# Optimization experiments

Measured on AMD Instinct MI355X. Metric: run time of the kernel, lower is better.

## Reference

```python
import jax, jax.numpy as jnp
import numpy as np

N = 100000
E = 1600000
K = 2  # KProp steps


def setup_inputs() -> dict:
    key = jax.random.key(0)
    ks = jax.random.split(key, 8)
    x = jax.random.normal(ks[0], (N, 64), dtype=jnp.float32)
    edge_index = jax.random.randint(ks[1], (2, E), 0, N, dtype=jnp.int32)
    s = 1.0 / np.sqrt(64)
    W2l = jax.random.normal(ks[2], (64, 64), dtype=jnp.float32) * s
    W2r = jax.random.normal(ks[3], (64, 64), dtype=jnp.float32) * s
    b2 = jnp.zeros((64,), dtype=jnp.float32)
    W3l = jax.random.normal(ks[4], (64, 16), dtype=jnp.float32) * s
    W3r = jax.random.normal(ks[5], (64, 16), dtype=jnp.float32) * s
    b3 = jnp.zeros((16,), dtype=jnp.float32)
    return {"x": x, "edge_index": edge_index, "W2l": W2l, "W2r": W2r,
            "b2": b2, "W3l": W3l, "W3r": W3r, "b3": b3}


def reference(x, edge_index, W2l, W2r, b2, W3l, W3r, b3):
    dst, src = edge_index[0], edge_index[1]  # adj_t[i,j]: edge j -> i
    ones = jnp.ones((E,), dtype=x.dtype)
    deg = jax.ops.segment_sum(ones, dst, num_segments=N)  # in-degree
    dinv = jnp.where(deg > 0, jax.lax.rsqrt(jnp.maximum(deg, 1.0)), 0.0)
    w = dinv[dst] * dinv[src]  # gcn_norm weights (no self-loops in norm)

    # KProp: K steps of (D^-1/2 A D^-1/2 + I) @ h  (set_diag adds unit diag)
    h = x
    for _ in range(K):
        h = jax.ops.segment_sum(w[:, None] * h[src], dst, num_segments=N) + h

    degm = jnp.maximum(deg, 1.0)[:, None]

    # SAGEConv 1: mean-neighbor aggregate + root weight
    agg = jax.ops.segment_sum(h[src], dst, num_segments=N) / degm
    h = agg @ W2l + h @ W2r + b2
    h = jax.nn.selu(h)

    # SAGEConv 2
    agg = jax.ops.segment_sum(h[src], dst, num_segments=N) / degm
    h = agg @ W3l + h @ W3r + b3
    return jax.nn.softmax(h, axis=1)
```

## Files before the change

### kernel.cpp

```cpp
#include <hip/hip_runtime.h>
#include <hip/hip_bf16.h>

#define NNODES 100000
#define NEDGES 1600000
#define NC 25
#define CAP1 68000
#define NBUCK 391
#define BCAP 4800
#define SPLIT_TILE 2048
#define NSPLIT ((NEDGES + SPLIT_TILE - 1) / SPLIT_TILE)
#define T2TILES 17

typedef short short8 __attribute__((ext_vector_type(8)));
typedef unsigned short ushx8 __attribute__((ext_vector_type(8)));
typedef float floatx4 __attribute__((ext_vector_type(4)));

__device__ __forceinline__ unsigned short f2b(float f) {
    unsigned u = __float_as_uint(f);
    u += 0x7fffu + ((u >> 16) & 1u);
    return (unsigned short)(u >> 16);
}

__device__ __forceinline__ void acc8(float* a, ushx8 u) {
#pragma unroll
    for (int i = 0; i < 8; ++i)
        a[i] += __uint_as_float((unsigned)u[i] << 16);
}

__global__ __launch_bounds__(256) void split1_kernel(
    const int* __restrict__ dst, const int* __restrict__ src,
    int* __restrict__ gcur1, unsigned* __restrict__ cpairs) {
    __shared__ int lhist[NC];
    __shared__ int lstart[NC];
    __shared__ int ldst[SPLIT_TILE];
    int t = threadIdx.x;
    if (t < NC) lhist[t] = 0;
    __syncthreads();
    int base = blockIdx.x * SPLIT_TILE;
    int n = min(SPLIT_TILE, NEDGES - base);
    for (int i = t; i < n; i += 256) {
        int d = dst[base + i];
        ldst[i] = d;
        atomicAdd(&lhist[d >> 12], 1);
    }
    __syncthreads();
    if (t < NC) {
        int c = lhist[t];
        lstart[t] = (c > 0) ? atomicAdd(&gcur1[t], c) : 0;
        lhist[t] = 0;
    }
    __syncthreads();
    for (int i = t; i < n; i += 256) {
        int d = ldst[i];
        int k = d >> 12;
        int s = src[base + i];
        int pos = lstart[k] + atomicAdd(&lhist[k], 1);
        cpairs[(size_t)k * CAP1 + pos] = ((unsigned)s << 12) | (unsigned)(d & 4095);
    }
}

__global__ __launch_bounds__(256) void split2_kernel(
    const unsigned* __restrict__ cpairs, const int* __restrict__ gcur1,
    int* __restrict__ gcur2, unsigned* __restrict__ fpairs) {
    int c = blockIdx.x / T2TILES;
    int tile = blockIdx.x % T2TILES;
    int cnt = gcur1[c];
    int base = tile * 4096;
    if (base >= cnt) return;
    int n = min(4096, cnt - base);
    __shared__ unsigned stash[4096];
    __shared__ int lhist[16];
    __shared__ int lstart[16];
    int t = threadIdx.x;
    if (t < 16) lhist[t] = 0;
    __syncthreads();
    const unsigned* pb = cpairs + (size_t)c * CAP1 + base;
    for (int i = t; i < n; i += 256) {
        unsigned p = pb[i];
        stash[i] = p;
        atomicAdd(&lhist[(p >> 8) & 15], 1);
    }
    __syncthreads();
    if (t < 16) {
        int cc = lhist[t];
        lstart[t] = (cc > 0) ? atomicAdd(&gcur2[c * 16 + t], cc) : 0;
        lhist[t] = 0;
    }
    __syncthreads();
    for (int i = t; i < n; i += 256) {
        unsigned p = stash[i];
        int f = (p >> 8) & 15;
        int pos = lstart[f] + atomicAdd(&lhist[f], 1);
        fpairs[(size_t)(c * 16 + f) * BCAP + pos] = ((p >> 12) << 8) | (p & 255u);
    }
}

__global__ void bucketscan_kernel(const int* __restrict__ gcur2, int* __restrict__ basearr) {
    __shared__ int lds[512];
    int t = threadIdx.x;
    int v = (t < NBUCK) ? gcur2[t] : 0;
    lds[t] = v;
    __syncthreads();
    for (int s = 1; s < 512; s <<= 1) {
        int u = (t >= s) ? lds[t - s] : 0;
        __syncthreads();
        lds[t] += u;
        __syncthreads();
    }
    if (t < NBUCK) basearr[t] = lds[t] - v;
}

__global__ __launch_bounds__(256) void finalize_kernel(
    const unsigned* __restrict__ fpairs, const int* __restrict__ gcur2,
    const int* __restrict__ basearr, const float* __restrict__ x,
    int* __restrict__ col, int* __restrict__ deg, int* __restrict__ rowoff,
    float* __restrict__ dinv, unsigned short* __restrict__ g0b) {
    __shared__ int ldeg[256];
    __shared__ int lcur[256];
    __shared__ float ldi[256];
    __shared__ int lsc[256];
    int k = blockIdx.x;
    int t = threadIdx.x;
    int node0 = k << 8;
    int ncount = min(256, NNODES - node0);
    int base = basearr[k];
    int count = gcur2[k];
    ldeg[t] = 0;
    __syncthreads();
    const unsigned* pb = fpairs + (size_t)k * BCAP;
    for (int i = t; i < count; i += 256) {
        atomicAdd(&ldeg[pb[i] & 255], 1);
    }
    __syncthreads();
    int a = ldeg[t];
    lsc[t] = a;
    __syncthreads();
    for (int s = 1; s < 256; s <<= 1) {
        int v = (t >= s) ? lsc[t - s] : 0;
        __syncthreads();
        lsc[t] += v;
        __syncthreads();
    }
    int excl = lsc[t] - a;
    lcur[t] = base + excl;
    if (t < ncount) {
        int n0 = node0 + t;
        rowoff[n0] = base + excl;
        deg[n0] = a;
        float di = (a > 0) ? rsqrtf((float)a) : 0.0f;
        ldi[t] = di;
        dinv[n0] = di;
    }
    __syncthreads();
    for (int i = t; i < count; i += 256) {
        unsigned p = pb[i];
        int dl = (int)(p & 255u);
        int s = (int)(p >> 8);
        int pos = atomicAdd(&lcur[dl], 1);
        col[pos] = s;
    }
    const float4* x4 = (const float4*)x;
    int f4count = ncount * 16;
    int b4 = node0 * 16;
    for (int j = t; j < f4count; j += 256) {
        float di = ldi[j >> 4];
        float4 v = x4[b4 + j];
        ushort4 u;
        u.x = f2b(di * v.x); u.y = f2b(di * v.y);
        u.z = f2b(di * v.z); u.w = f2b(di * v.w);
        *(ushort4*)(g0b + (size_t)(b4 + j) * 4) = u;
    }
}

template <int MODE>
__global__ __launch_bounds__(256) void gatherw_kernel(
    const unsigned short* __restrict__ vin, const float* __restrict__ hinf,
    const unsigned short* __restrict__ hinb,
    unsigned short* __restrict__ out0, unsigned short* __restrict__ out1,
    const int* __restrict__ rowoff, const int* __restrict__ deg,
    const int* __restrict__ col, const float* __restrict__ dinv) {
    int node = blockIdx.x * 4 + (threadIdx.x >> 6);
    int lane = threadIdx.x & 63;
    int sub = lane & 7;
    int g = lane >> 3;
    int beg = rowoff[node];
    int dg = deg[node];
    int end = beg + dg;
    float af[8] = {0.f, 0.f, 0.f, 0.f, 0.f, 0.f, 0.f, 0.f};
    float bf[8] = {0.f, 0.f, 0.f, 0.f, 0.f, 0.f, 0.f, 0.f};
    int e = beg + g;
    for (; e + 8 < end; e += 16) {
        int c0 = col[e];
        int c1 = col[e + 8];
        ushx8 u0 = *(const ushx8*)(vin + (size_t)c0 * 64 + sub * 8);
        ushx8 u1 = *(const ushx8*)(vin + (size_t)c1 * 64 + sub * 8);
        acc8(af, u0);
        acc8(bf, u1);
    }
    if (e < end) {
        int c0 = col[e];
        ushx8 u0 = *(const ushx8*)(vin + (size_t)c0 * 64 + sub * 8);
        acc8(af, u0);
    }
#pragma unroll
    for (int i = 0; i < 8; ++i) {
        float v = af[i] + bf[i];
        v += __shfl_xor(v, 8);
        v += __shfl_xor(v, 16);
        v += __shfl_xor(v, 32);
        af[i] = v;
    }
    if (lane < 8) {
        size_t off = (size_t)node * 64 + lane * 8;
        if (MODE <= 1) {
            float di = dinv[node];
            float hv[8];
            if (MODE == 0) {
                float4 h0 = *(const float4*)(hinf + off);
                float4 h1 = *(const float4*)(hinf + off + 4);
                hv[0] = h0.x; hv[1] = h0.y; hv[2] = h0.z; hv[3] = h0.w;
                hv[4] = h1.x; hv[5] = h1.y; hv[6] = h1.z; hv[7] = h1.w;
            } else {
                ushx8 u = *(const ushx8*)(hinb + off);
#pragma unroll
                for (int i = 0; i < 8; ++i) hv[i] = __uint_as_float((unsigned)u[i] << 16);
            }
            ushx8 uh, ug;
#pragma unroll
            for (int i = 0; i < 8; ++i) {
                float hn = hv[i] + di * af[i];
                uh[i] = f2b(hn);
                if (MODE == 0) ug[i] = f2b(di * hn);
            }
            *(ushx8*)(out0 + off) = uh;
            if (MODE == 0) *(ushx8*)(out1 + off) = ug;
        } else {
            float r = 1.0f / (float)(dg > 0 ? dg : 1);
            ushx8 u;
#pragma unroll
            for (int i = 0; i < 8; ++i) u[i] = f2b(af[i] * r);
            *(ushx8*)(out0 + off) = u;
        }
    }
}

__global__ __launch_bounds__(256) void dense1_mfma(
    const unsigned short* __restrict__ aggb, const unsigned short* __restrict__ hb,
    unsigned short* __restrict__ h3b,
    const float* __restrict__ W2l, const float* __restrict__ W2r,
    const float* __restrict__ b2) {
    __shared__ unsigned short Wt[64 * 144];
    int t = threadIdx.x;
    for (int idx = t; idx < 128 * 64; idx += 256) {
        int k = idx >> 6, j = idx & 63;
        float v = (k < 64) ? W2l[k * 64 + j] : W2r[(k - 64) * 64 + j];
        Wt[j * 144 + k] = f2b(v);
    }
    __syncthreads();
    int wib = t >> 6, lane = t & 63;
    int tile = blockIdx.x * 4 + wib;
    if (tile * 16 >= NNODES) return;
    int node0 = tile * 16;
    int jj = lane & 15, kg = lane >> 4;
    short8 bfrag[4][4];
#pragma unroll
    for (int nt = 0; nt < 4; ++nt)
#pragma unroll
        for (int s = 0; s < 4; ++s)
            bfrag[nt][s] = *(const short8*)&Wt[(nt * 16 + jj) * 144 + s * 32 + kg * 8];
    int arow = node0 + jj;
    const unsigned short* ap = aggb + (size_t)arow * 64 + kg * 8;
    const unsigned short* hp = hb + (size_t)arow * 64 + kg * 8;
    short8 afrag[4];
    afrag[0] = *(const short8*)ap;
    afrag[1] = *(const short8*)(ap + 32);
    afrag[2] = *(const short8*)hp;
    afrag[3] = *(const short8*)(hp + 32);
    const float lam = 1.0507009873554804934193349852946f;
    const float alp = 1.6732632423543772848170429916717f;
#pragma unroll
    for (int nt = 0; nt < 4; ++nt) {
        floatx4 acc = {0.f, 0.f, 0.f, 0.f};
#pragma unroll
        for (int s = 0; s < 4; ++s)
            acc = __builtin_amdgcn_mfma_f32_16x16x32_bf16(afrag[s], bfrag[nt][s], acc, 0, 0, 0);
        float bias = b2[nt * 16 + jj];
#pragma unroll
        for (int r = 0; r < 4; ++r) {
            float v = acc[r] + bias;
            float o = (v > 0.0f) ? lam * v : lam * alp * expm1f(v);
            int node = node0 + kg * 4 + r;
            h3b[(size_t)node * 64 + nt * 16 + jj] = f2b(o);
        }
    }
}

__global__ __launch_bounds__(256) void dense2_mfma(
    const unsigned short* __restrict__ aggb, const unsigned short* __restrict__ hb,
    float* __restrict__ out,
    const float* __restrict__ W3l, const float* __restrict__ W3r,
    const float* __restrict__ b3) {
    __shared__ unsigned short Wt[16 * 144];
    int t = threadIdx.x;
    for (int idx = t; idx < 128 * 16; idx += 256) {
        int k = idx >> 4, j = idx & 15;
        float v = (k < 64) ? W3l[k * 16 + j] : W3r[(k - 64) * 16 + j];
        Wt[j * 144 + k] = f2b(v);
    }
    __syncthreads();
    int wib = t >> 6, lane = t & 63;
    int tile = blockIdx.x * 4 + wib;
    if (tile * 16 >= NNODES) return;
    int node0 = tile * 16;
    int jj = lane & 15, kg = lane >> 4;
    short8 bfrag[4];
#pragma unroll
    for (int s = 0; s < 4; ++s)
        bfrag[s] = *(const short8*)&Wt[jj * 144 + s * 32 + kg * 8];
    int arow = node0 + jj;
    const unsigned short* ap = aggb + (size_t)arow * 64 + kg * 8;
    const unsigned short* hp = hb + (size_t)arow * 64 + kg * 8;
    short8 afrag[4];
    afrag[0] = *(const short8*)ap;
    afrag[1] = *(const short8*)(ap + 32);
    afrag[2] = *(const short8*)hp;
    afrag[3] = *(const short8*)(hp + 32);
    floatx4 acc = {0.f, 0.f, 0.f, 0.f};
#pragma unroll
    for (int s = 0; s < 4; ++s)
        acc = __builtin_amdgcn_mfma_f32_16x16x32_bf16(afrag[s], bfrag[s], acc, 0, 0, 0);
    float bias = b3[jj];
#pragma unroll
    for (int r = 0; r < 4; ++r) {
        float v = acc[r] + bias;
        float m = v;
        m = fmaxf(m, __shfl_xor(m, 1));
        m = fmaxf(m, __shfl_xor(m, 2));
        m = fmaxf(m, __shfl_xor(m, 4));
        m = fmaxf(m, __shfl_xor(m, 8));
        float ex = expf(v - m);
        float s2 = ex;
        s2 += __shfl_xor(s2, 1);
        s2 += __shfl_xor(s2, 2);
        s2 += __shfl_xor(s2, 4);
        s2 += __shfl_xor(s2, 8);
        int node = node0 + kg * 4 + r;
        out[(size_t)node * 16 + jj] = ex / s2;
    }
}

extern "C" void kernel_launch(void* const* d_in, const int* in_sizes, int n_in,
                              void* d_out, int out_size, void* d_ws, size_t ws_size,
                              hipStream_t stream) {
    const float* x   = (const float*)d_in[0];
    const int*   ei  = (const int*)d_in[1];
    const float* W2l = (const float*)d_in[2];
    const float* W2r = (const float*)d_in[3];
    const float* b2  = (const float*)d_in[4];
    const float* W3l = (const float*)d_in[5];
    const float* W3r = (const float*)d_in[6];
    const float* b3  = (const float*)d_in[7];
    float* out = (float*)d_out;

    const int* dst = ei;
    const int* src = ei + NEDGES;

    char* ws = (char*)d_ws;
    unsigned short* B0 = (unsigned short*)ws; ws += (size_t)NNODES * 64 * 2;
    unsigned short* B1 = (unsigned short*)ws; ws += (size_t)NNODES * 64 * 2;
    unsigned short* B2 = (unsigned short*)ws; ws += (size_t)NNODES * 64 * 2;
    int*      col     = (int*)ws;      ws += (size_t)NEDGES * 4;
    int*      deg     = (int*)ws;      ws += (size_t)NNODES * 4;
    int*      rowoff  = (int*)ws;      ws += (size_t)NNODES * 4;
    float*    dinv    = (float*)ws;    ws += (size_t)NNODES * 4;
    int*      gcur1   = (int*)ws;      ws += NC * 4;
    int*      gcur2   = (int*)ws;      ws += NBUCK * 4;
    int*      basearr = (int*)ws;      ws += NBUCK * 4;

    unsigned* cpairs = (unsigned*)B1;
    unsigned* fpairs = (unsigned*)B2;

    hipMemsetAsync(gcur1, 0, (NC + NBUCK) * 4, stream);

    split1_kernel<<<NSPLIT, 256, 0, stream>>>(dst, src, gcur1, cpairs);
    split2_kernel<<<NC * T2TILES, 256, 0, stream>>>(cpairs, gcur1, gcur2, fpairs);
    bucketscan_kernel<<<1, 512, 0, stream>>>(gcur2, basearr);
    finalize_kernel<<<NBUCK, 256, 0, stream>>>(fpairs, gcur2, basearr, x,
                                               col, deg, rowoff, dinv, B0);

    int nblk = NNODES / 4;
    int ndense = (NNODES / 16 + 3) / 4;
    gatherw_kernel<0><<<nblk, 256, 0, stream>>>(B0, x, nullptr, B1, B2, rowoff, deg, col, dinv);
    gatherw_kernel<1><<<nblk, 256, 0, stream>>>(B2, nullptr, B1, B0, nullptr, rowoff, deg, col, dinv);
    gatherw_kernel<2><<<nblk, 256, 0, stream>>>(B0, nullptr, nullptr, B1, nullptr, rowoff, deg, col, dinv);
    dense1_mfma<<<ndense, 256, 0, stream>>>(B1, B0, B2, W2l, W2r, b2);
    gatherw_kernel<2><<<nblk, 256, 0, stream>>>(B2, nullptr, nullptr, B0, nullptr, rowoff, deg, col, dinv);
    dense2_mfma<<<ndense, 256, 0, stream>>>(B0, B2, out, W3l, W3r, b3);
}
```

Before: 327.7 us.

## Fuse SAGE mean aggregation into MFMA dense kernels and warp-aggregate split2 atomics

Each wavefront now gathers the mean-neighbor aggregate for its 16-node tile into LDS and feeds it straight into the MFMA dense layer. This removes the separate gather kernels and the global round trip of the aggregate buffer for both SAGE layers. split2 now uses ballot-based per-wave ranking instead of per-element LDS atomics. The trade-off is that each wave processes 16 nodes serially, which lowers gather parallelism and may expose latency. The LDS sync relies on an s_waitcnt rather than a barrier, which is valid only because the data stays within one wave.

Measured after the change: 383.4 us. +17.0%, slower.

```diff
diff --git a/kernel.cpp b/kernel.cpp
--- a/kernel.cpp
+++ b/kernel.cpp
@@ -10,6 +10,7 @@
 #define SPLIT_TILE 2048
 #define NSPLIT ((NEDGES + SPLIT_TILE - 1) / SPLIT_TILE)
 #define T2TILES 17
+#define NTILES (NNODES / 16)
 
 typedef short short8 __attribute__((ext_vector_type(8)));
 typedef unsigned short ushx8 __attribute__((ext_vector_type(8)));
@@ -71,27 +72,57 @@
     __shared__ unsigned stash[4096];
     __shared__ int lhist[16];
     __shared__ int lstart[16];
+    __shared__ int chunkbase[64][16];
     int t = threadIdx.x;
+    int lane = t & 63;
+    int w = t >> 6;
     if (t < 16) lhist[t] = 0;
     __syncthreads();
     const unsigned* pb = cpairs + (size_t)c * CAP1 + base;
-    for (int i = t; i < n; i += 256) {
-        unsigned p = pb[i];
-        stash[i] = p;
-        atomicAdd(&lhist[(p >> 8) & 15], 1);
+    int nchunk = (n + 63) >> 6;
+    for (int ch = w; ch < nchunk; ch += 4) {
+        int i = ch * 64 + lane;
+        unsigned p = 0;
+        int f = -1;
+        if (i < n) {
+            p = pb[i];
+            stash[i] = p;
+            f = (int)((p >> 8) & 15u);
+        }
+#pragma unroll
+        for (int b = 0; b < 16; ++b) {
+            unsigned long long m = __ballot(f == b);
+            if (lane == b) {
+                int cb = __popcll(m);
+                chunkbase[ch][b] = (cb > 0) ? atomicAdd(&lhist[b], cb) : 0;
+            }
+        }
     }
     __syncthreads();
     if (t < 16) {
         int cc = lhist[t];
         lstart[t] = (cc > 0) ? atomicAdd(&gcur2[c * 16 + t], cc) : 0;
-        lhist[t] = 0;
-    }
-    __syncthreads();
-    for (int i = t; i < n; i += 256) {
-        unsigned p = stash[i];
-        int f = (p >> 8) & 15;
-        int pos = lstart[f] + atomicAdd(&lhist[f], 1);
-        fpairs[(size_t)(c * 16 + f) * BCAP + pos] = ((p >> 12) << 8) | (p & 255u);
+    }
+    __syncthreads();
+    for (int ch = w; ch < nchunk; ch += 4) {
+        int i = ch * 64 + lane;
+        unsigned p = 0;
+        int f = -1;
+        if (i < n) {
+            p = stash[i];
+            f = (int)((p >> 8) & 15u);
+        }
+        unsigned long long lt = (1ull << lane) - 1ull;
+        int myrank = 0;
+#pragma unroll
+        for (int b = 0; b < 16; ++b) {
+            unsigned long long m = __ballot(f == b);
+            if (f == b) myrank = __popcll(m & lt);
+        }
+        if (i < n) {
+            int pos = lstart[f] + chunkbase[ch][f] + myrank;
+            fpairs[(size_t)(c * 16 + f) * BCAP + pos] = ((p >> 12) << 8) | (p & 255u);
+        }
     }
 }
 
@@ -212,78 +243,109 @@
     }
     if (lane < 8) {
         size_t off = (size_t)node * 64 + lane * 8;
-        if (MODE <= 1) {
-            float di = dinv[node];
-            float hv[8];
-            if (MODE == 0) {
-                float4 h0 = *(const float4*)(hinf + off);
-                float4 h1 = *(const float4*)(hinf + off + 4);
-                hv[0] = h0.x; hv[1] = h0.y; hv[2] = h0.z; hv[3] = h0.w;
-                hv[4] = h1.x; hv[5] = h1.y; hv[6] = h1.z; hv[7] = h1.w;
-            } else {
-                ushx8 u = *(const ushx8*)(hinb + off);
-#pragma unroll
-                for (int i = 0; i < 8; ++i) hv[i] = __uint_as_float((unsigned)u[i] << 16);
-            }
-            ushx8 uh, ug;
-#pragma unroll
-            for (int i = 0; i < 8; ++i) {
-                float hn = hv[i] + di * af[i];
-                uh[i] = f2b(hn);
-                if (MODE == 0) ug[i] = f2b(di * hn);
-            }
-            *(ushx8*)(out0 + off) = uh;
-            if (MODE == 0) *(ushx8*)(out1 + off) = ug;
+        float di = dinv[node];
+        float hv[8];
+        if (MODE == 0) {
+            float4 h0 = *(const float4*)(hinf + off);
+            float4 h1 = *(const float4*)(hinf + off + 4);
+            hv[0] = h0.x; hv[1] = h0.y; hv[2] = h0.z; hv[3] = h0.w;
+            hv[4] = h1.x; hv[5] = h1.y; hv[6] = h1.z; hv[7] = h1.w;
         } else {
-            float r = 1.0f / (float)(dg > 0 ? dg : 1);
-            ushx8 u;
-#pragma unroll
-            for (int i = 0; i < 8; ++i) u[i] = f2b(af[i] * r);
-            *(ushx8*)(out0 + off) = u;
-        }
-    }
-}
-
-__global__ __launch_bounds__(256) void dense1_mfma(
-    const unsigned short* __restrict__ aggb, const unsigned short* __restrict__ hb,
+            ushx8 u = *(const ushx8*)(hinb + off);
+#pragma unroll
+            for (int i = 0; i < 8; ++i) hv[i] = __uint_as_float((unsigned)u[i] << 16);
+        }
+        ushx8 uh, ug;
+#pragma unroll
+        for (int i = 0; i < 8; ++i) {
+            float hn = hv[i] + di * af[i];
+            uh[i] = f2b(hn);
+            if (MODE == 0) ug[i] = f2b(di * hn);
+        }
+        *(ushx8*)(out0 + off) = uh;
+        if (MODE == 0) *(ushx8*)(out1 + off) = ug;
+    }
+}
+
+__global__ __launch_bounds__(256) void aggdense1_kernel(
+    const unsigned short* __restrict__ hb,
     unsigned short* __restrict__ h3b,
     const float* __restrict__ W2l, const float* __restrict__ W2r,
-    const float* __restrict__ b2) {
-    __shared__ unsigned short Wt[64 * 144];
+    const float* __restrict__ b2,
+    const int* __restrict__ rowoff, const int* __restrict__ deg,
+    const int* __restrict__ col) {
+    __shared__ unsigned short Wt[64 * 136];
+    __shared__ unsigned short aggT[4][16 * 68];
     int t = threadIdx.x;
     for (int idx = t; idx < 128 * 64; idx += 256) {
         int k = idx >> 6, j = idx & 63;
         float v = (k < 64) ? W2l[k * 64 + j] : W2r[(k - 64) * 64 + j];
-        Wt[j * 144 + k] = f2b(v);
-    }
-    __syncthreads();
-    int wib = t >> 6, lane = t & 63;
-    int tile = blockIdx.x * 4 + wib;
-    if (tile * 16 >= NNODES) return;
+        Wt[j * 136 + k] = f2b(v);
+    }
+    __syncthreads();
+    int w = t >> 6, lane = t & 63;
+    int tile = blockIdx.x * 4 + w;
+    if (tile >= NTILES) return;
     int node0 = tile * 16;
+    int sub = lane & 7;
+    int g = lane >> 3;
+    for (int n = 0; n < 16; ++n) {
+        int node = node0 + n;
+        int beg = rowoff[node];
+        int dg = deg[node];
+        int end = beg + dg;
+        float af[8] = {0.f, 0.f, 0.f, 0.f, 0.f, 0.f, 0.f, 0.f};
+        float bf[8] = {0.f, 0.f, 0.f, 0.f, 0.f, 0.f, 0.f, 0.f};
+        int e = beg + g;
+        for (; e + 8 < end; e += 16) {
+            int c0 = col[e];
+            int c1 = col[e + 8];
+            ushx8 u0 = *(const ushx8*)(hb + (size_t)c0 * 64 + sub * 8);
+            ushx8 u1 = *(const ushx8*)(hb + (size_t)c1 * 64 + sub * 8);
+            acc8(af, u0);
+            acc8(bf, u1);
+        }
+        if (e < end) {
+            int c0 = col[e];
+            ushx8 u0 = *(const ushx8*)(hb + (size_t)c0 * 64 + sub * 8);
+            acc8(af, u0);
+        }
+#pragma unroll
+        for (int i = 0; i < 8; ++i) {
+            float v = af[i] + bf[i];
+            v += __shfl_xor(v, 8);
+            v += __shfl_xor(v, 16);
+            v += __shfl_xor(v, 32);
+            af[i] = v;
+        }
+        if (lane < 8) {
+            float r = 1.0f / (float)(dg > 0 ? dg : 1);
+            ushx8 u;
+#pragma unroll
+            for (int i = 0; i < 8; ++i) u[i] = f2b(af[i] * r);
+            *(ushx8*)&aggT[w][n * 68 + lane * 8] = u;
+        }
+    }
+    asm volatile("s_waitcnt lgkmcnt(0)" ::: "memory");
     int jj = lane & 15, kg = lane >> 4;
-    short8 bfrag[4][4];
-#pragma unroll
-    for (int nt = 0; nt < 4; ++nt)
-#pragma unroll
-        for (int s = 0; s < 4; ++s)
-            bfrag[nt][s] = *(const short8*)&Wt[(nt * 16 + jj) * 144 + s * 32 + kg * 8];
-    int arow = node0 + jj;
-    const unsigned short* ap = aggb + (size_t)arow * 64 + kg * 8;
-    const unsigned short* hp = hb + (size_t)arow * 64 + kg * 8;
     short8 afrag[4];
-    afrag[0] = *(const short8*)ap;
-    afrag[1] = *(const short8*)(ap + 32);
+    afrag[0] = *(const short8*)&aggT[w][jj * 68 + kg * 8];
+    afrag[1] = *(const short8*)&aggT[w][jj * 68 + 32 + kg * 8];
+    const unsigned short* hp = hb + (size_t)(node0 + jj) * 64 + kg * 8;
     afrag[2] = *(const short8*)hp;
     afrag[3] = *(const short8*)(hp + 32);
     const float lam = 1.0507009873554804934193349852946f;
     const float alp = 1.6732632423543772848170429916717f;
 #pragma unroll
     for (int nt = 0; nt < 4; ++nt) {
+        short8 bfrag[4];
+#pragma unroll
+        for (int s = 0; s < 4; ++s)
+            bfrag[s] = *(const short8*)&Wt[(nt * 16 + jj) * 136 + s * 32 + kg * 8];
         floatx4 acc = {0.f, 0.f, 0.f, 0.f};
 #pragma unroll
         for (int s = 0; s < 4; ++s)
-            acc = __builtin_amdgcn_mfma_f32_16x16x32_bf16(afrag[s], bfrag[nt][s], acc, 0, 0, 0);
+            acc = __builtin_amdgcn_mfma_f32_16x16x32_bf16(afrag[s], bfrag[s], acc, 0, 0, 0);
         float bias = b2[nt * 16 + jj];
 #pragma unroll
         for (int r = 0; r < 4; ++r) {
@@ -295,36 +357,77 @@
     }
 }
 
-__global__ __launch_bounds__(256) void dense2_mfma(
-    const unsigned short* __restrict__ aggb, const unsigned short* __restrict__ hb,
+__global__ __launch_bounds__(256) void aggdense2_kernel(
+    const unsigned short* __restrict__ hb,
     float* __restrict__ out,
     const float* __restrict__ W3l, const float* __restrict__ W3r,
-    const float* __restrict__ b3) {
-    __shared__ unsigned short Wt[16 * 144];
+    const float* __restrict__ b3,
+    const int* __restrict__ rowoff, const int* __restrict__ deg,
+    const int* __restrict__ col) {
+    __shared__ unsigned short Wt[16 * 136];
+    __shared__ unsigned short aggT[4][16 * 68];
     int t = threadIdx.x;
     for (int idx = t; idx < 128 * 16; idx += 256) {
         int k = idx >> 4, j = idx & 15;
         float v = (k < 64) ? W3l[k * 16 + j] : W3r[(k - 64) * 16 + j];
-        Wt[j * 144 + k] = f2b(v);
-    }
-    __syncthreads();
-    int wib = t >> 6, lane = t & 63;
-    int tile = blockIdx.x * 4 + wib;
-    if (tile * 16 >= NNODES) return;
+        Wt[j * 136 + k] = f2b(v);
+    }
+    __syncthreads();
+    int w = t >> 6, lane = t & 63;
+    int tile = blockIdx.x * 4 + w;
+    if (tile >= NTILES) return;
     int node0 = tile * 16;
+    int sub = lane & 7;
+    int g = lane >> 3;
+    for (int n = 0; n < 16; ++n) {
+        int node = node0 + n;
+        int beg = rowoff[node];
+        int dg = deg[node];
+        int end = beg + dg;
+        float af[8] = {0.f, 0.f, 0.f, 0.f, 0.f, 0.f, 0.f, 0.f};
+        float bf[8] = {0.f, 0.f, 0.f, 0.f, 0.f, 0.f, 0.f, 0.f};
+        int e = beg + g;
+        for (; e + 8 < end; e += 16) {
+            int c0 = col[e];
+            int c1 = col[e + 8];
+            ushx8 u0 = *(const ushx8*)(hb + (size_t)c0 * 64 + sub * 8);
+            ushx8 u1 = *(const ushx8*)(hb + (size_t)c1 * 64 + sub * 8);
+            acc8(af, u0);
+            acc8(bf, u1);
+        }
+        if (e < end) {
+            int c0 = col[e];
+            ushx8 u0 = *(const ushx8*)(hb + (size_t)c0 * 64 + sub * 8);
+            acc8(af, u0);
+        }
+#pragma unroll
+        for (int i = 0; i < 8; ++i) {
+            float v = af[i] + bf[i];
+            v += __shfl_xor(v, 8);
+            v += __shfl_xor(v, 16);
+            v += __shfl_xor(v, 32);
+            af[i] = v;
+        }
+        if (lane < 8) {
+            float r = 1.0f / (float)(dg > 0 ? dg : 1);
+            ushx8 u;
+#pragma unroll
+            for (int i = 0; i < 8; ++i) u[i] = f2b(af[i] * r);
+            *(ushx8*)&aggT[w][n * 68 + lane * 8] = u;
+        }
+    }
+    asm volatile("s_waitcnt lgkmcnt(0)" ::: "memory");
     int jj = lane & 15, kg = lane >> 4;
-    short8 bfrag[4];
-#pragma unroll
-    for (int s = 0; s < 4; ++s)
-        bfrag[s] = *(const short8*)&Wt[jj * 144 + s * 32 + kg * 8];
-    int arow = node0 + jj;
-    const unsigned short* ap = aggb + (size_t)arow * 64 + kg * 8;
-    const unsigned short* hp = hb + (size_t)arow * 64 + kg * 8;
     short8 afrag[4];
-    afrag[0] = *(const short8*)ap;
-    afrag[1] = *(const short8*)(ap + 32);
+    afrag[0] = *(const short8*)&aggT[w][jj * 68 + kg * 8];
+    afrag[1] = *(const short8*)&aggT[w][jj * 68 + 32 + kg * 8];
+    const unsigned short* hp = hb + (size_t)(node0 + jj) * 64 + kg * 8;
     afrag[2] = *(const short8*)hp;
     afrag[3] = *(const short8*)(hp + 32);
+    short8 bfrag[4];
+#pragma unroll
+    for (int s = 0; s < 4; ++s)
+        bfrag[s] = *(const short8*)&Wt[jj * 136 + s * 32 + kg * 8];
     floatx4 acc = {0.f, 0.f, 0.f, 0.f};
 #pragma unroll
     for (int s = 0; s < 4; ++s)
@@ -379,6 +482,7 @@
 
     unsigned* cpairs = (unsigned*)B1;
     unsigned* fpairs = (unsigned*)B2;
+    unsigned short* h3b = B2;
 
     hipMemsetAsync(gcur1, 0, (NC + NBUCK) * 4, stream);
 
@@ -389,11 +493,9 @@
                                                col, deg, rowoff, dinv, B0);
 
     int nblk = NNODES / 4;
-    int ndense = (NNODES / 16 + 3) / 4;
+    int nfused = (NTILES + 3) / 4;
     gatherw_kernel<0><<<nblk, 256, 0, stream>>>(B0, x, nullptr, B1, B2, rowoff, deg, col, dinv);
     gatherw_kernel<1><<<nblk, 256, 0, stream>>>(B2, nullptr, B1, B0, nullptr, rowoff, deg, col, dinv);
-    gatherw_kernel<2><<<nblk, 256, 0, stream>>>(B0, nullptr, nullptr, B1, nullptr, rowoff, deg, col, dinv);
-    dense1_mfma<<<ndense, 256, 0, stream>>>(B1, B0, B2, W2l, W2r, b2);
-    gatherw_kernel<2><<<nblk, 256, 0, stream>>>(B2, nullptr, nullptr, B0, nullptr, rowoff, deg, col, dinv);
-    dense2_mfma<<<ndense, 256, 0, stream>>>(B0, B2, out, W3l, W3r, b3);
-}
+    aggdense1_kernel<<<nfused, 256, 0, stream>>>(B0, h3b, W2l, W2r, b2, rowoff, deg, col);
+    aggdense2_kernel<<<nfused, 256, 0, stream>>>(h3b, out, W3l, W3r, b3, rowoff, deg, col);
+}
```

## Fold bucket scan into finalize and drop second scaled output in first propagation

Applied to the files above, without the earlier changes.

Removes the separate single-block bucket scan kernel by having every finalize block recompute the prefix over bucket counts in shared memory. The first propagation step no longer writes a second dinv-scaled bf16 copy; the second step instead loads dinv per neighbour and scales on the fly, cutting one full-size write at the cost of extra scattered 4-byte loads per edge. Split tile size is also doubled, halving the number of split1 blocks.

Result: no change. 324.7 us (-0.9%).

```diff
diff --git a/kernel.cpp b/kernel.cpp
--- a/kernel.cpp
+++ b/kernel.cpp
@@ -7,9 +7,10 @@
 #define CAP1 68000
 #define NBUCK 391
 #define BCAP 4800
-#define SPLIT_TILE 2048
+#define SPLIT_TILE 4096
 #define NSPLIT ((NEDGES + SPLIT_TILE - 1) / SPLIT_TILE)
 #define T2TILES 17
+#define NTILES (NNODES / 16)
 
 typedef short short8 __attribute__((ext_vector_type(8)));
 typedef unsigned short ushx8 __attribute__((ext_vector_type(8)));
@@ -25,6 +26,12 @@
 #pragma unroll
     for (int i = 0; i < 8; ++i)
         a[i] += __uint_as_float((unsigned)u[i] << 16);
+}
+
+__device__ __forceinline__ void acc8s(float* a, ushx8 u, float s) {
+#pragma unroll
+    for (int i = 0; i < 8; ++i)
+        a[i] = fmaf(s, __uint_as_float((unsigned)u[i] << 16), a[i]);
 }
 
 __global__ __launch_bounds__(256) void split1_kernel(
@@ -95,38 +102,38 @@
     }
 }
 
-__global__ void bucketscan_kernel(const int* __restrict__ gcur2, int* __restrict__ basearr) {
-    __shared__ int lds[512];
-    int t = threadIdx.x;
-    int v = (t < NBUCK) ? gcur2[t] : 0;
-    lds[t] = v;
-    __syncthreads();
-    for (int s = 1; s < 512; s <<= 1) {
-        int u = (t >= s) ? lds[t - s] : 0;
-        __syncthreads();
-        lds[t] += u;
-        __syncthreads();
-    }
-    if (t < NBUCK) basearr[t] = lds[t] - v;
-}
-
 __global__ __launch_bounds__(256) void finalize_kernel(
     const unsigned* __restrict__ fpairs, const int* __restrict__ gcur2,
-    const int* __restrict__ basearr, const float* __restrict__ x,
+    const float* __restrict__ x,
     int* __restrict__ col, int* __restrict__ deg, int* __restrict__ rowoff,
     float* __restrict__ dinv, unsigned short* __restrict__ g0b) {
     __shared__ int ldeg[256];
     __shared__ int lcur[256];
     __shared__ float ldi[256];
     __shared__ int lsc[256];
+    __shared__ int bb[NBUCK + 1];
     int k = blockIdx.x;
     int t = threadIdx.x;
+    int a2 = (2 * t < NBUCK) ? gcur2[2 * t] : 0;
+    int b2v = (2 * t + 1 < NBUCK) ? gcur2[2 * t + 1] : 0;
+    int ts = a2 + b2v;
+    lsc[t] = ts;
+    __syncthreads();
+    for (int s = 1; s < 256; s <<= 1) {
+        int v = (t >= s) ? lsc[t - s] : 0;
+        __syncthreads();
+        lsc[t] += v;
+        __syncthreads();
+    }
+    int excl2 = lsc[t] - ts;
+    if (2 * t < NBUCK) bb[2 * t] = excl2;
+    if (2 * t + 1 < NBUCK) bb[2 * t + 1] = excl2 + a2;
+    ldeg[t] = 0;
+    __syncthreads();
     int node0 = k << 8;
     int ncount = min(256, NNODES - node0);
-    int base = basearr[k];
+    int base = bb[k];
     int count = gcur2[k];
-    ldeg[t] = 0;
-    __syncthreads();
     const unsigned* pb = fpairs + (size_t)k * BCAP;
     for (int i = t; i < count; i += 256) {
         atomicAdd(&ldeg[pb[i] & 255], 1);
@@ -176,7 +183,7 @@
 __global__ __launch_bounds__(256) void gatherw_kernel(
     const unsigned short* __restrict__ vin, const float* __restrict__ hinf,
     const unsigned short* __restrict__ hinb,
-    unsigned short* __restrict__ out0, unsigned short* __restrict__ out1,
+    unsigned short* __restrict__ out0,
     const int* __restrict__ rowoff, const int* __restrict__ deg,
     const int* __restrict__ col, const float* __restrict__ dinv) {
     int node = blockIdx.x * 4 + (threadIdx.x >> 6);
@@ -194,13 +201,25 @@
         int c1 = col[e + 8];
         ushx8 u0 = *(const ushx8*)(vin + (size_t)c0 * 64 + sub * 8);
         ushx8 u1 = *(const ushx8*)(vin + (size_t)c1 * 64 + sub * 8);
-        acc8(af, u0);
-        acc8(bf, u1);
+        if (MODE == 1) {
+            float d0 = dinv[c0];
+            float d1 = dinv[c1];
+            acc8s(af, u0, d0);
+            acc8s(bf, u1, d1);
+        } else {
+            acc8(af, u0);
+            acc8(bf, u1);
+        }
     }
     if (e < end) {
         int c0 = col[e];
         ushx8 u0 = *(const ushx8*)(vin + (size_t)c0 * 64 + sub * 8);
-        acc8(af, u0);
+        if (MODE == 1) {
+            float d0 = dinv[c0];
+            acc8s(af, u0, d0);
+        } else {
+            acc8(af, u0);
+        }
     }
 #pragma unroll
     for (int i = 0; i < 8; ++i) {
@@ -212,6 +231,7 @@
     }
     if (lane < 8) {
         size_t off = (size_t)node * 64 + lane * 8;
+        ushx8 uh;
         if (MODE <= 1) {
             float di = dinv[node];
             float hv[8];
@@ -225,22 +245,14 @@
 #pragma unroll
                 for (int i = 0; i < 8; ++i) hv[i] = __uint_as_float((unsigned)u[i] << 16);
             }
-            ushx8 uh, ug;
-#pragma unroll
-            for (int i = 0; i < 8; ++i) {
-                float hn = hv[i] + di * af[i];
-                uh[i] = f2b(hn);
-                if (MODE == 0) ug[i] = f2b(di * hn);
-            }
-            *(ushx8*)(out0 + off) = uh;
-            if (MODE == 0) *(ushx8*)(out1 + off) = ug;
+#pragma unroll
+            for (int i = 0; i < 8; ++i) uh[i] = f2b(hv[i] + di * af[i]);
         } else {
             float r = 1.0f / (float)(dg > 0 ? dg : 1);
-            ushx8 u;
-#pragma unroll
-            for (int i = 0; i < 8; ++i) u[i] = f2b(af[i] * r);
-            *(ushx8*)(out0 + off) = u;
+#pragma unroll
+            for (int i = 0; i < 8; ++i) uh[i] = f2b(af[i] * r);
         }
+        *(ushx8*)(out0 + off) = uh;
     }
 }
 
@@ -259,7 +271,7 @@
     __syncthreads();
     int wib = t >> 6, lane = t & 63;
     int tile = blockIdx.x * 4 + wib;
-    if (tile * 16 >= NNODES) return;
+    if (tile >= NTILES) return;
     int node0 = tile * 16;
     int jj = lane & 15, kg = lane >> 4;
     short8 bfrag[4][4];
@@ -310,7 +322,7 @@
     __syncthreads();
     int wib = t >> 6, lane = t & 63;
     int tile = blockIdx.x * 4 + wib;
-    if (tile * 16 >= NNODES) return;
+    if (tile >= NTILES) return;
     int node0 = tile * 16;
     int jj = lane & 15, kg = lane >> 4;
     short8 bfrag[4];
@@ -375,25 +387,26 @@
     float*    dinv    = (float*)ws;    ws += (size_t)NNODES * 4;
     int*      gcur1   = (int*)ws;      ws += NC * 4;
     int*      gcur2   = (int*)ws;      ws += NBUCK * 4;
-    int*      basearr = (int*)ws;      ws += NBUCK * 4;
 
     unsigned* cpairs = (unsigned*)B1;
     unsigned* fpairs = (unsigned*)B2;
+    unsigned short* h1b = B1;
+    unsigned short* h2b = B0;
+    unsigned short* h3b = B1;
 
     hipMemsetAsync(gcur1, 0, (NC + NBUCK) * 4, stream);
 
     split1_kernel<<<NSPLIT, 256, 0, stream>>>(dst, src, gcur1, cpairs);
     split2_kernel<<<NC * T2TILES, 256, 0, stream>>>(cpairs, gcur1, gcur2, fpairs);
-    bucketscan_kernel<<<1, 512, 0, stream>>>(gcur2, basearr);
-    finalize_kernel<<<NBUCK, 256, 0, stream>>>(fpairs, gcur2, basearr, x,
+    finalize_kernel<<<NBUCK, 256, 0, stream>>>(fpairs, gcur2, x,
                                                col, deg, rowoff, dinv, B0);
 
     int nblk = NNODES / 4;
-    int ndense = (NNODES / 16 + 3) / 4;
-    gatherw_kernel<0><<<nblk, 256, 0, stream>>>(B0, x, nullptr, B1, B2, rowoff, deg, col, dinv);
-    gatherw_kernel<1><<<nblk, 256, 0, stream>>>(B2, nullptr, B1, B0, nullptr, rowoff, deg, col, dinv);
-    gatherw_kernel<2><<<nblk, 256, 0, stream>>>(B0, nullptr, nullptr, B1, nullptr, rowoff, deg, col, dinv);
-    dense1_mfma<<<ndense, 256, 0, stream>>>(B1, B0, B2, W2l, W2r, b2);
-    gatherw_kernel<2><<<nblk, 256, 0, stream>>>(B2, nullptr, nullptr, B0, nullptr, rowoff, deg, col, dinv);
-    dense2_mfma<<<ndense, 256, 0, stream>>>(B0, B2, out, W3l, W3r, b3);
-}
+    int ndense = (NTILES + 3) / 4;
+    gatherw_kernel<0><<<nblk, 256, 0, stream>>>(B0, x, nullptr, h1b, rowoff, deg, col, dinv);
+    gatherw_kernel<1><<<nblk, 256, 0, stream>>>(h1b, nullptr, h1b, h2b, rowoff, deg, col, dinv);
+    gatherw_kernel<2><<<nblk, 256, 0, stream>>>(h2b, nullptr, nullptr, B2, rowoff, deg, col, dinv);
+    dense1_mfma<<<ndense, 256, 0, stream>>>(B2, h2b, h3b, W2l, W2r, b2);
+    gatherw_kernel<2><<<nblk, 256, 0, stream>>>(h3b, nullptr, nullptr, B2, rowoff, deg, col, dinv);
+    dense2_mfma<<<ndense, 256, 0, stream>>>(B2, h3b, out, W3l, W3r, b3);
+}
```
